# Kernel tuning notes

Hardware: AMD Instinct MI355X
Metric: run time of the kernel (lower is better)

Reference implementation:

```python
import jax, jax.numpy as jnp
import numpy as np

B, H, S, D = 1, 16, 8192, 64
WINDOW = 1024  # window_size from init; also used as the query block size


def setup_inputs() -> dict:
    key = jax.random.key(0)
    kq, kk, kv = jax.random.split(key, 3)
    Q = jax.random.normal(kq, (B, H, S, D), dtype=jnp.float32)
    K = jax.random.normal(kk, (B, H, S, D), dtype=jnp.float32)
    V = jax.random.normal(kv, (B, H, S, D), dtype=jnp.float32)
    return {"Q": Q, "K": K, "V": V}


def _sliding_window_attn(Q, K, V, window):
    # Banded causal attention: query q attends kv with 0 <= q - kv <= window.
    # Tile queries into blocks of size W=window; each query block i only needs
    # kv positions [i*W - W, i*W + W), i.e. a 2W-wide local slice. This honors
    # the block-sparse structure instead of materializing an SxS score matrix.
    b, h, s, d = Q.shape
    W = window
    nb = s // W  # number of query blocks
    # Pad K,V by W zeros at the front so every block slice is in-bounds.
    Kp = jnp.pad(K, ((0, 0), (0, 0), (W, 0), (0, 0)))
    Vp = jnp.pad(V, ((0, 0), (0, 0), (W, 0), (0, 0)))
    # Local kv indices for each block: block i covers padded positions [i*W, i*W+2W).
    idx = jnp.arange(nb)[:, None] * W + jnp.arange(2 * W)[None, :]  # [nb, 2W]
    Kb = Kp[:, :, idx, :]  # [B,H,nb,2W,D]
    Vb = Vp[:, :, idx, :]  # [B,H,nb,2W,D]
    Qb = Q.reshape(b, h, nb, W, d)  # [B,H,nb,W,D]

    scale = np.float32(1.0 / np.sqrt(d))  # flex_attention default scaling
    scores = jnp.einsum('bhnqd,bhnkd->bhnqk', Qb, Kb) * scale  # [B,H,nb,W,2W]

    # Global positions: q_global = i*W + qi ; kv_global = i*W + kj - W.
    # Mask conds: q>=kv  <=> qi >= kj - W ;  q-kv<=W  <=> qi <= kj ; kv_global>=0.
    qi = jnp.arange(W)[:, None]          # [W,1]
    kj = jnp.arange(2 * W)[None, :]      # [1,2W]
    rel_mask = (qi <= kj) & (qi >= kj - W)                        # [W,2W]
    kv_global = jnp.arange(nb)[:, None, None] * W + kj[None] - W  # [nb,1,2W]
    mask = rel_mask[None] & (kv_global >= 0)                      # [nb,W,2W]

    neg = jnp.finfo(scores.dtype).min
    scores = jnp.where(mask[None, None], scores, neg)
    attn = jax.nn.softmax(scores, axis=-1)
    out = jnp.einsum('bhnqk,bhnkd->bhnqd', attn, Vb)
    return out.reshape(b, h, s, d)


def reference(Q, K, V):
    return _sliding_window_attn(Q, K, V, WINDOW)
```

## Files before the change

kernel.cpp:

```cpp
#include <hip/hip_runtime.h>
#include <stdint.h>

namespace {
constexpr int kH = 16;
constexpr int kS = 8192;
constexpr int kD = 64;
constexpr int kW = 1024;

typedef __attribute__((ext_vector_type(4)))  float float4_t;
typedef __attribute__((ext_vector_type(16))) float f32x16;
typedef __attribute__((ext_vector_type(8)))  short bf16x8;
typedef __attribute__((ext_vector_type(8)))  short short8_t;

__device__ __forceinline__ unsigned short f2bf(float f) {
    union { float fv; uint32_t u; } c; c.fv = f;
    return (unsigned short)((c.u + 0x7fffu + ((c.u >> 16) & 1u)) >> 16);
}

__device__ __forceinline__ float fexp2(float x) {
#if __has_builtin(__builtin_amdgcn_exp2f)
    return __builtin_amdgcn_exp2f(x);
#else
    return exp2f(x);
#endif
}

__device__ __forceinline__ void gload16(const void* g, char* l) {
    __builtin_amdgcn_global_load_lds(
        (const __attribute__((address_space(1))) void*)g,
        (__attribute__((address_space(3))) void*)l, 16, 0, 0);
}

__global__ __launch_bounds__(256)
void prep_kv(const float* __restrict__ K, const float* __restrict__ V,
             unsigned short* __restrict__ Kb, unsigned short* __restrict__ Vt) {
    __shared__ float tile[64][65];
    const int h  = blockIdx.y;
    const int s0 = blockIdx.x * 64;
    const int tid = threadIdx.x;
    const size_t hb = (size_t)h * kS * kD;

    {
        const size_t base = hb + (size_t)s0 * kD + (size_t)tid * 16;
        float4_t a = *(const float4_t*)(K + base);
        float4_t b = *(const float4_t*)(K + base + 4);
        float4_t c = *(const float4_t*)(K + base + 8);
        float4_t d = *(const float4_t*)(K + base + 12);
        short8_t o0, o1;
        #pragma unroll
        for (int j = 0; j < 4; ++j) {
            o0[j] = (short)f2bf(a[j]); o0[j + 4] = (short)f2bf(b[j]);
            o1[j] = (short)f2bf(c[j]); o1[j + 4] = (short)f2bf(d[j]);
        }
        *(short8_t*)(Kb + base)     = o0;
        *(short8_t*)(Kb + base + 8) = o1;
    }

    #pragma unroll
    for (int it = 0; it < 4; ++it) {
        const int n = tid + it * 256;
        const int s = n >> 4, d0 = (n & 15) * 4;
        float4_t v = *(const float4_t*)(V + hb + (size_t)(s0 + s) * kD + d0);
        tile[s][d0 + 0] = v[0]; tile[s][d0 + 1] = v[1];
        tile[s][d0 + 2] = v[2]; tile[s][d0 + 3] = v[3];
    }
    __syncthreads();
    #pragma unroll
    for (int it = 0; it < 2; ++it) {
        const int n = tid + it * 256;
        const int d = n >> 3, sc = (n & 7) * 8;
        short8_t o;
        #pragma unroll
        for (int j = 0; j < 8; ++j) o[j] = (short)f2bf(tile[sc + j][d]);
        *(short8_t*)(Vt + (size_t)h * kD * kS + (size_t)d * kS + s0 + sc) = o;
    }
}

__global__ __launch_bounds__(256, 4)
void swa_main(const float* __restrict__ Qg, const unsigned short* __restrict__ Kb,
              const unsigned short* __restrict__ Vt, float* __restrict__ Og) {
    __shared__ __align__(16) char lds[2][16384];

    const int lid  = blockIdx.x;
    const int swz  = (lid & 7) * 128 + (lid >> 3);
    const int h    = swz >> 6;
    const int qblk = swz & 63;

    const int tid  = threadIdx.x;
    const int wv   = tid >> 6;
    const int lane = tid & 63;
    const int lq   = lane & 31;
    const int hi   = lane >> 5;

    const int q0b = qblk * 128;
    const int qs  = q0b + wv * 32;
    const int q   = qs + lq;
    const size_t hb  = (size_t)h * kS * kD;
    const size_t hbv = (size_t)h * kD * kS;

    constexpr float qscale = 0.125f * 1.44269504f;
    bf16x8 qf[4];
    {
        const float* qp = Qg + hb + (size_t)q * kD + hi * 8;
        #pragma unroll
        for (int c = 0; c < 4; ++c) {
            float4_t a = *(const float4_t*)(qp + c * 16);
            float4_t b = *(const float4_t*)(qp + c * 16 + 4);
            bf16x8 f;
            #pragma unroll
            for (int j = 0; j < 4; ++j) {
                f[j]     = (short)f2bf(a[j] * qscale);
                f[j + 4] = (short)f2bf(b[j] * qscale);
            }
            qf[c] = f;
        }
    }

    f32x16 acc[2], lsum;
    #pragma unroll
    for (int r = 0; r < 16; ++r) { acc[0][r] = 0.f; acc[1][r] = 0.f; lsum[r] = 0.f; }

    bf16x8 ones;
    #pragma unroll
    for (int j = 0; j < 8; ++j) ones[j] = (short)0x3F80;

    const int kstart = (q0b >= kW) ? q0b - kW : 0;
    const int nt     = (q0b + 128 - kstart) >> 6;

    int srcK[2], srcV[2];
    #pragma unroll
    for (int i = 0; i < 2; ++i) {
        const int n = tid + i * 256;
        const int c = n ^ ((n >> 3) & 7);
        srcK[i] = (c >> 3) * 64 + (c & 7) * 8;
        srcV[i] = (c >> 3) * kS + (c & 7) * 8;
    }
    const unsigned short* KbH = Kb + hb;
    const unsigned short* VtH = Vt + hbv;

    auto stage = [&](int buf, int kb) {
        const unsigned short* Kt = KbH + (size_t)kb * 64;
        const unsigned short* Vq = VtH + kb;
        #pragma unroll
        for (int i = 0; i < 2; ++i) {
            const int db = i * 4096 + wv * 1024;
            gload16(Kt + srcK[i], &lds[buf][db]);
            gload16(Vq + srcV[i], &lds[buf][8192 + db]);
        }
    };

    stage(0, kstart);
    for (int t = 0; t < nt; ++t) {
        const int kb  = kstart + t * 64;
        const int kbn = (t + 1 < nt) ? kb + 64 : kb;

        asm volatile("s_waitcnt vmcnt(0)" ::: "memory");
        __builtin_amdgcn_s_barrier();
        asm volatile("" ::: "memory");
        stage((t + 1) & 1, kbn);

        const char* Kl = lds[t & 1];
        const char* Vl = lds[t & 1] + 8192;

        #pragma unroll
        for (int half = 0; half < 2; ++half) {
            const int kh = kb + half * 32;
            if (kh <= qs && kh >= qs - kW) {
                const int krow = half * 32 + lq;
                const int ksw  = (krow & 7) << 4;
                bf16x8 kf[4];
                #pragma unroll
                for (int c = 0; c < 4; ++c)
                    kf[c] = *(const bf16x8*)(Kl + ((krow * 128 + c * 32 + hi * 16) ^ ksw));

                f32x16 st;
                #pragma unroll
                for (int r = 0; r < 16; ++r) st[r] = 0.f;
                __builtin_amdgcn_s_setprio(1);
                #pragma unroll
                for (int c = 0; c < 4; ++c)
                    st = __builtin_amdgcn_mfma_f32_32x32x16_bf16(kf[c], qf[c], st, 0, 0, 0);
                __builtin_amdgcn_s_setprio(0);

                const int vsw = (lq & 7) << 4;
                bf16x8 vf[4];
                #pragma unroll
                for (int dh = 0; dh < 2; ++dh)
                    #pragma unroll
                    for (int kc = 0; kc < 2; ++kc)
                        vf[dh * 2 + kc] = *(const bf16x8*)(
                            Vl + (((dh * 32 + lq) * 128 + half * 64 + kc * 32 + hi * 16) ^ vsw));

                float p[16];
                const bool interior = (kh <= qs - 32) && (kh >= qs - 992);
                if (interior) {
                    #pragma unroll
                    for (int r = 0; r < 16; ++r) p[r] = fexp2(st[r]);
                } else {
                    #pragma unroll
                    for (int r = 0; r < 16; ++r) {
                        const int ki = kh + (r & 3) + 8 * (r >> 2) + 4 * hi;
                        const bool ok = (ki <= q) && (ki + kW >= q);
                        const float e = fexp2(st[r]);
                        p[r] = ok ? e : 0.f;
                    }
                }

                unsigned int wrd[8];
                #pragma unroll
                for (int j = 0; j < 8; ++j)
                    asm("v_cvt_pk_bf16_f32 %0, %1, %2" : "=v"(wrd[j]) : "v"(p[2 * j]), "v"(p[2 * j + 1]));
                asm("v_permlane32_swap_b32 %0, %1" : "+v"(wrd[0]), "+v"(wrd[2]));
                asm("v_permlane32_swap_b32 %0, %1" : "+v"(wrd[1]), "+v"(wrd[3]));
                asm("v_permlane32_swap_b32 %0, %1" : "+v"(wrd[4]), "+v"(wrd[6]));
                asm("v_permlane32_swap_b32 %0, %1" : "+v"(wrd[5]), "+v"(wrd[7]));
                union U { unsigned int u[4]; bf16x8 v; };
                U u0, u1;
                u0.u[0] = wrd[0]; u0.u[1] = wrd[1]; u0.u[2] = wrd[2]; u0.u[3] = wrd[3];
                u1.u[0] = wrd[4]; u1.u[1] = wrd[5]; u1.u[2] = wrd[6]; u1.u[3] = wrd[7];

                __builtin_amdgcn_s_setprio(1);
                acc[0] = __builtin_amdgcn_mfma_f32_32x32x16_bf16(vf[0], u0.v, acc[0], 0, 0, 0);
                acc[1] = __builtin_amdgcn_mfma_f32_32x32x16_bf16(vf[2], u0.v, acc[1], 0, 0, 0);
                lsum   = __builtin_amdgcn_mfma_f32_32x32x16_bf16(ones,  u0.v, lsum,   0, 0, 0);
                acc[0] = __builtin_amdgcn_mfma_f32_32x32x16_bf16(vf[1], u1.v, acc[0], 0, 0, 0);
                acc[1] = __builtin_amdgcn_mfma_f32_32x32x16_bf16(vf[3], u1.v, acc[1], 0, 0, 0);
                lsum   = __builtin_amdgcn_mfma_f32_32x32x16_bf16(ones,  u1.v, lsum,   0, 0, 0);
                __builtin_amdgcn_s_setprio(0);
            }
        }
    }

    const float rl = 1.f / lsum[0];
    float* op = Og + hb + (size_t)q * kD;
    #pragma unroll
    for (int g = 0; g < 4; ++g) {
        float4_t o0, o1;
        #pragma unroll
        for (int j = 0; j < 4; ++j) {
            o0[j] = acc[0][g * 4 + j] * rl;
            o1[j] = acc[1][g * 4 + j] * rl;
        }
        *(float4_t*)(op + g * 8 + hi * 4)      = o0;
        *(float4_t*)(op + 32 + g * 8 + hi * 4) = o1;
    }
}
}

extern "C" void kernel_launch(void* const* d_in, const int* in_sizes, int n_in,
                              void* d_out, int out_size, void* d_ws, size_t ws_size,
                              hipStream_t stream) {
    (void)in_sizes; (void)n_in; (void)out_size; (void)ws_size;
    const float* Q = (const float*)d_in[0];
    const float* K = (const float*)d_in[1];
    const float* V = (const float*)d_in[2];
    float* O = (float*)d_out;
    unsigned short* Kb = (unsigned short*)d_ws;
    unsigned short* Vt = Kb + (size_t)kH * kS * kD;

    prep_kv<<<dim3(kS / 64, kH), dim3(256), 0, stream>>>(K, V, Kb, Vt);
    swa_main<<<dim3(1024), dim3(256), 0, stream>>>(Q, Kb, Vt, O);
}
```

Before: 78.23 us.

## Double query tile to 256 rows with 512-thread blocks and prefetch-before-wait pipeline

Each block now handles 256 queries with 8 waves, so every staged K/V tile in LDS is reused by twice as many query rows and the grid shrinks to 512 blocks. The prefetch of the next tile is issued before waiting on the current one (vmcnt(2)), and a second barrier at the end of each iteration protects the buffer being overwritten. The trade-offs are an extra barrier per tile, more wasted masked iterations per larger block, and fewer blocks, which can leave fewer waves available to hide latency.

New measurement: 79.72 us. No clear change (+1.9%).

```diff
diff --git a/kernel.cpp b/kernel.cpp
--- a/kernel.cpp
+++ b/kernel.cpp
@@ -76,15 +76,15 @@
     }
 }
 
-__global__ __launch_bounds__(256, 4)
+__global__ __launch_bounds__(512, 2)
 void swa_main(const float* __restrict__ Qg, const unsigned short* __restrict__ Kb,
               const unsigned short* __restrict__ Vt, float* __restrict__ Og) {
     __shared__ __align__(16) char lds[2][16384];
 
     const int lid  = blockIdx.x;
-    const int swz  = (lid & 7) * 128 + (lid >> 3);
-    const int h    = swz >> 6;
-    const int qblk = swz & 63;
+    const int swz  = (lid & 7) * 64 + (lid >> 3);
+    const int h    = swz >> 5;
+    const int qblk = swz & 31;
 
     const int tid  = threadIdx.x;
     const int wv   = tid >> 6;
@@ -92,7 +92,7 @@
     const int lq   = lane & 31;
     const int hi   = lane >> 5;
 
-    const int q0b = qblk * 128;
+    const int q0b = qblk * 256;
     const int qs  = q0b + wv * 32;
     const int q   = qs + lq;
     const size_t hb  = (size_t)h * kS * kD;
@@ -125,39 +125,30 @@
     for (int j = 0; j < 8; ++j) ones[j] = (short)0x3F80;
 
     const int kstart = (q0b >= kW) ? q0b - kW : 0;
-    const int nt     = (q0b + 128 - kstart) >> 6;
-
-    int srcK[2], srcV[2];
-    #pragma unroll
-    for (int i = 0; i < 2; ++i) {
-        const int n = tid + i * 256;
-        const int c = n ^ ((n >> 3) & 7);
-        srcK[i] = (c >> 3) * 64 + (c & 7) * 8;
-        srcV[i] = (c >> 3) * kS + (c & 7) * 8;
+    const int nt     = (q0b + 256 - kstart) >> 6;
+
+    int srcK, srcV;
+    {
+        const int c = tid ^ ((tid >> 3) & 7);
+        srcK = (c >> 3) * 64 + (c & 7) * 8;
+        srcV = (c >> 3) * kS + (c & 7) * 8;
     }
     const unsigned short* KbH = Kb + hb;
     const unsigned short* VtH = Vt + hbv;
 
     auto stage = [&](int buf, int kb) {
-        const unsigned short* Kt = KbH + (size_t)kb * 64;
-        const unsigned short* Vq = VtH + kb;
-        #pragma unroll
-        for (int i = 0; i < 2; ++i) {
-            const int db = i * 4096 + wv * 1024;
-            gload16(Kt + srcK[i], &lds[buf][db]);
-            gload16(Vq + srcV[i], &lds[buf][8192 + db]);
-        }
+        gload16(KbH + (size_t)kb * 64 + srcK, &lds[buf][tid * 16]);
+        gload16(VtH + kb + srcV,              &lds[buf][8192 + tid * 16]);
     };
 
     stage(0, kstart);
     for (int t = 0; t < nt; ++t) {
         const int kb  = kstart + t * 64;
         const int kbn = (t + 1 < nt) ? kb + 64 : kb;
-
-        asm volatile("s_waitcnt vmcnt(0)" ::: "memory");
+        stage((t + 1) & 1, kbn);
+        asm volatile("s_waitcnt vmcnt(2)" ::: "memory");
         __builtin_amdgcn_s_barrier();
         asm volatile("" ::: "memory");
-        stage((t + 1) & 1, kbn);
 
         const char* Kl = lds[t & 1];
         const char* Vl = lds[t & 1] + 8192;
@@ -167,7 +158,7 @@
             const int kh = kb + half * 32;
             if (kh <= qs && kh >= qs - kW) {
                 const int krow = half * 32 + lq;
-                const int ksw  = (krow & 7) << 4;
+                const int ksw  = (lq & 7) << 4;
                 bf16x8 kf[4];
                 #pragma unroll
                 for (int c = 0; c < 4; ++c)
@@ -182,14 +173,13 @@
                     st = __builtin_amdgcn_mfma_f32_32x32x16_bf16(kf[c], qf[c], st, 0, 0, 0);
                 __builtin_amdgcn_s_setprio(0);
 
-                const int vsw = (lq & 7) << 4;
                 bf16x8 vf[4];
                 #pragma unroll
                 for (int dh = 0; dh < 2; ++dh)
                     #pragma unroll
                     for (int kc = 0; kc < 2; ++kc)
                         vf[dh * 2 + kc] = *(const bf16x8*)(
-                            Vl + (((dh * 32 + lq) * 128 + half * 64 + kc * 32 + hi * 16) ^ vsw));
+                            Vl + (((dh * 32 + lq) * 128 + half * 64 + kc * 32 + hi * 16) ^ ksw));
 
                 float p[16];
                 const bool interior = (kh <= qs - 32) && (kh >= qs - 992);
@@ -229,6 +219,10 @@
                 __builtin_amdgcn_s_setprio(0);
             }
         }
+
+        asm volatile("" ::: "memory");
+        __builtin_amdgcn_s_barrier();
+        asm volatile("" ::: "memory");
     }
 
     const float rl = 1.f / lsum[0];
@@ -259,5 +253,5 @@
     unsigned short* Vt = Kb + (size_t)kH * kS * kD;
 
     prep_kv<<<dim3(kS / 64, kH), dim3(256), 0, stream>>>(K, V, Kb, Vt);
-    swa_main<<<dim3(1024), dim3(256), 0, stream>>>(Q, Kb, Vt, O);
-}
+    swa_main<<<dim3(512), dim3(512), 0, stream>>>(Q, Kb, Vt, O);
+}
```
